# Performance work log

Hardware: AMD Instinct MI355X
Metric: run time of the kernel (lower is better)

The kernel has to match this reference:

```python
import math
import jax, jax.numpy as jnp
import numpy as np

B, S, D, H, REL_V = 2, 2048, 1024, 16, 64
HD = D // H
EPS = 1e-5


def _layernorm(x, w, b):
    # torch-style: std with Bessel correction (unbiased), divide by (std + eps)
    u = x.mean(-1, keepdims=True)
    xc = x - u
    s = jnp.sqrt((xc * xc).sum(-1, keepdims=True) / (x.shape[-1] - 1))
    return w * (xc / (s + EPS)) + b


def _gelu(x):
    return 0.5 * x * (1 + jnp.tanh(math.sqrt(2 / math.pi) * (x + 0.044715 * x ** 3)))


def setup_inputs() -> dict:
    key = jax.random.key(0)
    ks = jax.random.split(key, 6)
    wscale = 0.02
    return {
        "x": jax.random.normal(ks[0], (B, S, D), jnp.float32),
        "rel": jax.random.randint(ks[1], (B, S, S), 0, REL_V, jnp.int32),
        "ln1_w": jnp.ones((D,), jnp.float32),
        "ln1_b": jnp.zeros((D,), jnp.float32),
        "Wqkv": jax.random.normal(ks[2], (D, 3 * D), jnp.float32) * wscale,
        "bqkv": jnp.zeros((3 * D,), jnp.float32),
        "Wo": jax.random.normal(ks[3], (D, D), jnp.float32) * wscale,
        "bo": jnp.zeros((D,), jnp.float32),
        "rel_emb": jax.random.normal(ks[4], (REL_V, H), jnp.float32) * wscale,
        "ln2_w": jnp.ones((D,), jnp.float32),
        "ln2_b": jnp.zeros((D,), jnp.float32),
        "Wfc": jax.random.normal(ks[5], (D, 4 * D), jnp.float32) * wscale,
        "bfc": jnp.zeros((4 * D,), jnp.float32),
        "Wp": jax.random.normal(jax.random.fold_in(key, 7), (4 * D, D), jnp.float32) * wscale,
        "bp": jnp.zeros((D,), jnp.float32),
    }


def reference(x, rel, ln1_w, ln1_b, Wqkv, bqkv, Wo, bo, rel_emb,
              ln2_w, ln2_b, Wfc, bfc, Wp, bp):
    h = _layernorm(x, ln1_w, ln1_b)
    qkv = h @ Wqkv + bqkv  # [B,S,3D]
    q, k, v = jnp.split(qkv, 3, axis=-1)
    q = q.reshape(B, S, H, HD).transpose(0, 2, 1, 3)  # [B,H,S,HD]
    k = k.reshape(B, S, H, HD).transpose(0, 2, 1, 3)
    v = v.reshape(B, S, H, HD).transpose(0, 2, 1, 3)

    w = jnp.einsum('bhqd,bhkd->bhqk', q, k) / math.sqrt(HD)  # scale=True
    mask = jnp.tril(jnp.ones((S, S), w.dtype))  # causal tril buffer
    w = w * mask - 1e10 * (1 - mask)
    # faithful to original: rel bias multiplies masked logits (zeroing masked -1e10)
    relw = rel_emb[rel]                    # [B,S,S,H]
    relw = relw.transpose(0, 3, 1, 2)      # [B,H,S,S]
    w = w * (relw * mask)
    p = jax.nn.softmax(w, axis=-1)
    a = jnp.einsum('bhqk,bhkd->bhqd', p, v)       # [B,H,S,HD]
    a = a.transpose(0, 2, 1, 3).reshape(B, S, D)  # merge heads
    a = a @ Wo + bo

    x = x + a
    m = _gelu(_layernorm(x, ln2_w, ln2_b) @ Wfc + bfc) @ Wp + bp
    return x + m
```

## Files before the change

kernel.cpp:

```cpp
#include <hip/hip_runtime.h>
#include <hip/hip_bf16.h>
#include <math.h>

using bf16 = __hip_bfloat16;
typedef __bf16 bf16x8 __attribute__((ext_vector_type(8)));
typedef float f32x4 __attribute__((ext_vector_type(4)));

#define SEQ 2048
#define DIM 1024
#define NH 16
#define HDIM 64
#define BATCH 2

__device__ __forceinline__ void load_lds16(const bf16* g, bf16* l) {
  __builtin_amdgcn_global_load_lds((__attribute__((address_space(1))) void*)g,
                                   (__attribute__((address_space(3))) void*)l, 16, 0, 0);
}

__global__ __launch_bounds__(256) void transpose_k(const float* __restrict__ in,
                                                   bf16* __restrict__ out, int R, int C) {
  __shared__ float tile[32][33];
  int c0 = blockIdx.x * 32, r0 = blockIdx.y * 32;
  int tx = threadIdx.x, ty = threadIdx.y;
#pragma unroll
  for (int j = 0; j < 4; ++j)
    tile[ty + 8 * j][tx] = in[(size_t)(r0 + ty + 8 * j) * C + c0 + tx];
  __syncthreads();
#pragma unroll
  for (int j = 0; j < 4; ++j)
    out[(size_t)(c0 + ty + 8 * j) * R + r0 + tx] = __float2bfloat16(tile[tx][ty + 8 * j]);
}

__global__ __launch_bounds__(256) void ln_k(const float* __restrict__ x,
                                            const float* __restrict__ w,
                                            const float* __restrict__ bb,
                                            bf16* __restrict__ out) {
  int row = blockIdx.x, tid = threadIdx.x;
  int wid = tid >> 6, lane = tid & 63;
  const float* xr = x + (size_t)row * DIM;
  float4 vv = *(const float4*)&xr[tid * 4];
  float v[4] = {vv.x, vv.y, vv.z, vv.w};
  float s = v[0] + v[1] + v[2] + v[3];
#pragma unroll
  for (int m = 1; m < 64; m <<= 1) s += __shfl_xor(s, m, 64);
  __shared__ float red[8];
  if (lane == 0) red[wid] = s;
  __syncthreads();
  float mean = (red[0] + red[1] + red[2] + red[3]) * (1.f / DIM);
  float q = 0.f;
#pragma unroll
  for (int j = 0; j < 4; ++j) {
    v[j] -= mean;
    q += v[j] * v[j];
  }
#pragma unroll
  for (int m = 1; m < 64; m <<= 1) q += __shfl_xor(q, m, 64);
  if (lane == 0) red[4 + wid] = q;
  __syncthreads();
  float ssq = red[4] + red[5] + red[6] + red[7];
  float sd = sqrtf(ssq / (float)(DIM - 1));
  float inv = 1.f / (sd + 1e-5f);
  float4 wv = *(const float4*)&w[tid * 4];
  float4 bv4 = *(const float4*)&bb[tid * 4];
  float wl[4] = {wv.x, wv.y, wv.z, wv.w};
  float bl[4] = {bv4.x, bv4.y, bv4.z, bv4.w};
  unsigned short pk[4];
#pragma unroll
  for (int j = 0; j < 4; ++j)
    pk[j] = __bfloat16_as_ushort(__float2bfloat16(wl[j] * (v[j] * inv) + bl[j]));
  *(uint2*)&out[(size_t)row * DIM + tid * 4] = *(uint2*)pk;
}

__global__ __launch_bounds__(512) void gemm256_k(
    const bf16* __restrict__ A, const bf16* __restrict__ Bt, const float* __restrict__ bias,
    int N, int K, int mode, bf16* __restrict__ o0, bf16* __restrict__ o1,
    bf16* __restrict__ o2) {
  __shared__ bf16 LDSb[65536];
  int tid = threadIdx.x;
  int wid = tid >> 6, lane = tid & 63, quad = lane >> 4, l15 = lane & 15;
  int wm = wid >> 2, wn = wid & 3;
  int m0 = blockIdx.y * 256, n0 = blockIdx.x * 256;
  int grow = lane >> 2;
  int gslot = (lane & 3) ^ ((lane >> 3) & 3);
  const int nt = K >> 6;

  float bv[4];
#pragma unroll
  for (int nf = 0; nf < 4; ++nf) bv[nf] = bias[n0 + wn * 64 + nf * 16 + l15];

  auto stageA = [&](int tile, int ks) {
    int bd = tile & 1;
#pragma unroll
    for (int it = 0; it < 2; ++it) {
      int c = wid * 2 + it;
      load_lds16(A + (size_t)(m0 + c * 16 + grow) * K + tile * 64 + ks * 32 + gslot * 8,
                 &LDSb[bd * 32768 + ks * 8192 + c * 512]);
    }
  };
  auto stageB = [&](int tile, int ks) {
    int bd = tile & 1;
#pragma unroll
    for (int it = 0; it < 2; ++it) {
      int c = wid * 2 + it;
      load_lds16(Bt + (size_t)(n0 + c * 16 + grow) * K + tile * 64 + ks * 32 + gslot * 8,
                 &LDSb[bd * 32768 + 16384 + ks * 8192 + c * 512]);
    }
  };

  f32x4 acc[8][4] = {};

  stageA(0, 0); stageB(0, 0);
  stageA(0, 1); stageB(0, 1);
  stageA(1, 0); stageB(1, 0);
  asm volatile("s_waitcnt vmcnt(8)" ::: "memory");
  __builtin_amdgcn_sched_barrier(0);
  __builtin_amdgcn_s_barrier();
  __builtin_amdgcn_sched_barrier(0);

#define PHASE(BD, KS, MH, STAGE_STMT, WAIT_STMT)                                             \
  {                                                                                          \
    bf16x8 af[4], bq[4];                                                                     \
    _Pragma("unroll") for (int j = 0; j < 4; ++j) {                                          \
      int r = wm * 128 + (MH) * 64 + j * 16 + l15;                                           \
      af[j] = *(const bf16x8*)&LDSb[(BD) * 32768 + (KS) * 8192 + (r >> 4) * 512 +            \
                                    (r & 15) * 32 + ((quad ^ ((r >> 1) & 3)) << 3)];         \
    }                                                                                        \
    _Pragma("unroll") for (int n = 0; n < 4; ++n) {                                          \
      int r = wn * 64 + n * 16 + l15;                                                        \
      bq[n] = *(const bf16x8*)&LDSb[(BD) * 32768 + 16384 + (KS) * 8192 + (r >> 4) * 512 +    \
                                    (r & 15) * 32 + ((quad ^ ((r >> 1) & 3)) << 3)];         \
    }                                                                                        \
    STAGE_STMT;                                                                              \
    __builtin_amdgcn_sched_barrier(0);                                                       \
    __builtin_amdgcn_s_barrier();                                                            \
    __builtin_amdgcn_sched_barrier(0);                                                       \
    __builtin_amdgcn_s_setprio(1);                                                           \
    _Pragma("unroll") for (int j = 0; j < 4; ++j)                                            \
        _Pragma("unroll") for (int n = 0; n < 4; ++n)                                        \
            acc[(MH) * 4 + j][n] = __builtin_amdgcn_mfma_f32_16x16x32_bf16(                  \
                af[j], bq[n], acc[(MH) * 4 + j][n], 0, 0, 0);                                \
    __builtin_amdgcn_s_setprio(0);                                                           \
    WAIT_STMT;                                                                               \
    __builtin_amdgcn_sched_barrier(0);                                                       \
    __builtin_amdgcn_s_barrier();                                                            \
    __builtin_amdgcn_sched_barrier(0);                                                       \
  }

  for (int t = 0; t < nt; ++t) {
    int bd = t & 1;
    PHASE(bd, 0, 0, { if (t + 1 < nt) stageA(t + 1, 1); }, {});
    PHASE(bd, 0, 1, { if (t + 1 < nt) stageB(t + 1, 1); }, {
      if (t + 1 < nt) asm volatile("s_waitcnt vmcnt(8)" ::: "memory");
      else            asm volatile("s_waitcnt vmcnt(0)" ::: "memory");
    });
    PHASE(bd, 1, 0, { if (t + 2 < nt) stageA(t + 2, 0); }, {});
    PHASE(bd, 1, 1, { if (t + 2 < nt) stageB(t + 2, 0); }, {
      if (t + 2 < nt)      asm volatile("s_waitcnt vmcnt(8)" ::: "memory");
      else if (t + 1 < nt) asm volatile("s_waitcnt vmcnt(4)" ::: "memory");
    });
  }
#undef PHASE

#pragma unroll
  for (int mf = 0; mf < 8; ++mf) {
#pragma unroll
    for (int nf = 0; nf < 4; ++nf) {
      int col = n0 + wn * 64 + nf * 16 + l15;
      int row_base = m0 + wm * 128 + mf * 16 + quad * 4;
      if (mode == 0) {
        int which = col >> 10, d = col & 1023, hh = d >> 6, dd = d & 63;
        int b = row_base >> 11, s2 = row_base & 2047;
        if (which == 2) {
          unsigned short pk[4];
#pragma unroll
          for (int r = 0; r < 4; ++r)
            pk[r] = __bfloat16_as_ushort(__float2bfloat16(acc[mf][nf][r] + bv[nf]));
          *(uint2*)&o2[(((size_t)b * NH + hh) * HDIM + dd) * SEQ + s2] = *(uint2*)pk;
        } else {
          bf16* dst = which == 0 ? o0 : o1;
#pragma unroll
          for (int r = 0; r < 4; ++r)
            dst[(((size_t)b * NH + hh) * SEQ + s2 + r) * HDIM + dd] =
                __float2bfloat16(acc[mf][nf][r] + bv[nf]);
        }
      } else {
#pragma unroll
        for (int r = 0; r < 4; ++r) {
          float t2 = acc[mf][nf][r] + bv[nf];
          float u = 0.7978845608028654f * (t2 + 0.044715f * t2 * t2 * t2);
          float g = t2 / (1.f + __expf(-2.f * u));
          o0[(size_t)(row_base + r) * N + col] = __float2bfloat16(g);
        }
      }
    }
  }
}

template <int TM>
__global__ __launch_bounds__(256) void gemm_k(
    const bf16* __restrict__ A, const bf16* __restrict__ Bt, const float* __restrict__ bias,
    int M, int N, int K, int mode,
    const float* __restrict__ residf, float* __restrict__ x2out, const float* __restrict__ x2in,
    float* __restrict__ outf) {
  constexpr int MT = TM / 32;
  constexpr int ACH = TM / 8;
  __shared__ bf16 As[TM * 64];
  __shared__ bf16 Bs[128 * 64];
  int tid = threadIdx.x;
  int wid = tid >> 6, lane = tid & 63, quad = lane >> 4, l15 = lane & 15;
  int wm = wid >> 1, wn = wid & 1;
  int m0 = blockIdx.y * TM, n0 = blockIdx.x * 128;
  int rsub = lane >> 3;
  int c8 = (lane & 7) ^ rsub;
  f32x4 acc[MT][4] = {};

  for (int k0 = 0; k0 < K; k0 += 64) {
    __syncthreads();
#pragma unroll
    for (int it = 0; it < ACH / 4; ++it) {
      int c = wid * (ACH / 4) + it;
      int row = c * 8 + rsub;
      load_lds16(A + (size_t)(m0 + row) * K + k0 + c8 * 8, &As[c * 512]);
    }
#pragma unroll
    for (int it = 0; it < 4; ++it) {
      int c = wid * 4 + it;
      int row = c * 8 + rsub;
      load_lds16(Bt + (size_t)(n0 + row) * K + k0 + c8 * 8, &Bs[c * 512]);
    }
    __syncthreads();
#pragma unroll
    for (int ks = 0; ks < 2; ++ks) {
      bf16x8 af[MT], bfr[4];
#pragma unroll
      for (int mt = 0; mt < MT; ++mt) {
        int r = wm * (MT * 16) + mt * 16 + l15;
        af[mt] = *(const bf16x8*)&As[r * 64 + ((ks * 4 + quad) ^ (r & 7)) * 8];
      }
#pragma unroll
      for (int nt2 = 0; nt2 < 4; ++nt2) {
        int r = wn * 64 + nt2 * 16 + l15;
        bfr[nt2] = *(const bf16x8*)&Bs[r * 64 + ((ks * 4 + quad) ^ (r & 7)) * 8];
      }
#pragma unroll
      for (int mt = 0; mt < MT; ++mt)
#pragma unroll
        for (int nt2 = 0; nt2 < 4; ++nt2)
          acc[mt][nt2] =
              __builtin_amdgcn_mfma_f32_16x16x32_bf16(af[mt], bfr[nt2], acc[mt][nt2], 0, 0, 0);
    }
  }

#pragma unroll
  for (int mt = 0; mt < MT; ++mt) {
#pragma unroll
    for (int nt = 0; nt < 4; ++nt) {
      int col = n0 + wn * 64 + nt * 16 + l15;
      float bvs = bias[col];
      int row_base = m0 + wm * (MT * 16) + mt * 16 + quad * 4;
#pragma unroll
      for (int r = 0; r < 4; ++r) {
        int row = row_base + r;
        float val = acc[mt][nt][r] + bvs;
        size_t i = (size_t)row * N + col;
        if (mode == 1) x2out[i] = residf[i] + val;
        else           outf[i] = x2in[i] + val;
      }
    }
  }
}

__global__ __launch_bounds__(256) void sufv_k(const bf16* __restrict__ vt,
                                              float* __restrict__ suf) {
  int row = blockIdx.x;
  const bf16* src = vt + (size_t)row * SEQ;
  float* dst = suf + (size_t)row * SEQ;
  int tid = threadIdx.x;
  float v[8];
  float s = 0.f;
#pragma unroll
  for (int j = 0; j < 8; ++j) {
    v[j] = __bfloat162float(src[tid * 8 + j]);
    s += v[j];
  }
  __shared__ float sc[256];
  sc[tid] = s;
  __syncthreads();
  for (int off = 1; off < 256; off <<= 1) {
    float add = (tid + off < 256) ? sc[tid + off] : 0.f;
    __syncthreads();
    sc[tid] += add;
    __syncthreads();
  }
  float run = (tid < 255) ? sc[tid + 1] : 0.f;
#pragma unroll
  for (int j = 7; j >= 0; --j) {
    dst[tid * 8 + j] = run;
    run += v[j];
  }
}

__device__ __forceinline__ int pswz(int row) { return (row & 7) ^ (((row >> 3) & 1) << 1); }

__global__ __launch_bounds__(256) void attn_k(const bf16* __restrict__ q,
                                              const bf16* __restrict__ k,
                                              const bf16* __restrict__ v,
                                              const int* __restrict__ rel,
                                              const float* __restrict__ rel_emb,
                                              const float* __restrict__ suf,
                                              bf16* __restrict__ out) {
  int h = blockIdx.x;
  int y = blockIdx.y;
  int b = blockIdx.z;
  int tid = threadIdx.x;
  int wid = tid >> 6, lane = tid & 63, quad = lane >> 4, l15 = lane & 15;

  __shared__ __align__(16) char SM[40960];
  bf16* Kb = (bf16*)SM;
  bf16* Vb = (bf16*)(SM + 16384);
  bf16* Ps = (bf16*)(SM + 32768);
  float(*SufLds)[68] = (float(*)[68])SM;

  const size_t bh = (size_t)b * NH + h;
  const bf16* kb0 = k + bh * SEQ * HDIM;
  const bf16* vt0 = v + bh * (size_t)HDIM * SEQ;

  float rv = 0.125f * rel_emb[lane * NH + h];

  int rsub = lane >> 3;
  int c8 = (lane & 7) ^ rsub;

  const int prow_w = wid * 16 + quad * 4;
  const int prow_r = wid * 16 + l15;
  const int psw_r = pswz(prow_r);

  for (int sub = 0; sub < 2; ++sub) {
    int qt = (sub == 0) ? (31 - y) : y;

    const bf16* qb = q + (bh * SEQ + (size_t)qt * 64) * HDIM;
    bf16x8 aq[2];
#pragma unroll
    for (int ks = 0; ks < 2; ++ks)
      aq[ks] = *(const bf16x8*)(qb + (size_t)(wid * 16 + l15) * HDIM + ks * 32 + quad * 8);

    __syncthreads();

#pragma unroll
    for (int it = 0; it < 2; ++it) {
      int c = wid * 2 + it;
      int row = c * 8 + rsub;
      load_lds16(kb0 + (size_t)row * HDIM + c8 * 8, &Kb[c * 512]);
      load_lds16(vt0 + (size_t)row * SEQ + c8 * 8, &Vb[c * 512]);
    }

    const int* relq = rel + (size_t)b * SEQ * SEQ + (size_t)qt * 64 * SEQ;
    const int* rp[4];
#pragma unroll
    for (int r = 0; r < 4; ++r) rp[r] = relq + (size_t)(wid * 16 + quad * 4 + r) * SEQ;

    int ridx[4][4];
#pragma unroll
    for (int nt = 0; nt < 4; ++nt)
#pragma unroll
      for (int r = 0; r < 4; ++r) ridx[nt][r] = rp[r][nt * 16 + l15];

    __syncthreads();

    const int q_base = qt * 64 + wid * 16 + quad * 4;
    float l_part[4] = {0.f, 0.f, 0.f, 0.f};
    f32x4 o_acc[4] = {};

    for (int kt = 0; kt < qt; ++kt) {
      int cur = kt & 1;
      int ridx2[4][4];
      {
        bf16* Kd = Kb + (cur ^ 1) * 4096;
        bf16* Vd = Vb + (cur ^ 1) * 4096;
#pragma unroll
        for (int it = 0; it < 2; ++it) {
          int c = wid * 2 + it;
          int row = c * 8 + rsub;
          load_lds16(kb0 + (size_t)((kt + 1) * 64 + row) * HDIM + c8 * 8, &Kd[c * 512]);
          load_lds16(vt0 + (size_t)row * SEQ + (kt + 1) * 64 + c8 * 8, &Vd[c * 512]);
        }
#pragma unroll
        for (int nt = 0; nt < 4; ++nt)
#pragma unroll
          for (int r = 0; r < 4; ++r) ridx2[nt][r] = rp[r][(kt + 1) * 64 + nt * 16 + l15];
      }

      const bf16* Ksb = Kb + cur * 4096;
      const bf16* Vtb = Vb + cur * 4096;

      f32x4 sacc[4] = {};
      __builtin_amdgcn_s_setprio(1);
#pragma unroll
      for (int ks = 0; ks < 2; ++ks) {
#pragma unroll
        for (int nt = 0; nt < 4; ++nt) {
          bf16x8 bfr =
              *(const bf16x8*)&Ksb[(nt * 16 + l15) * 64 + ((ks * 4 + quad) ^ (l15 & 7)) * 8];
          sacc[nt] = __builtin_amdgcn_mfma_f32_16x16x32_bf16(aq[ks], bfr, sacc[nt], 0, 0, 0);
        }
      }
      __builtin_amdgcn_s_setprio(0);

#pragma unroll
      for (int nt = 0; nt < 4; ++nt) {
#pragma unroll
        for (int r = 0; r < 4; ++r) {
          float m = __shfl(rv, ridx[nt][r], 64);
          float p = __expf(sacc[nt][r] * m);
          l_part[r] += p;
          int row = prow_w + r;
          int sw = (nt * 2 + (l15 >> 3)) ^ pswz(row);
          Ps[row * 64 + sw * 8 + (l15 & 7)] = __float2bfloat16(p);
        }
      }

      __builtin_amdgcn_s_setprio(1);
#pragma unroll
      for (int ks = 0; ks < 2; ++ks) {
        bf16x8 af = *(const bf16x8*)&Ps[prow_r * 64 + ((ks * 4 + quad) ^ psw_r) * 8];
#pragma unroll
        for (int nt = 0; nt < 4; ++nt) {
          bf16x8 bfr =
              *(const bf16x8*)&Vtb[(nt * 16 + l15) * 64 + ((ks * 4 + quad) ^ (l15 & 7)) * 8];
          o_acc[nt] = __builtin_amdgcn_mfma_f32_16x16x32_bf16(af, bfr, o_acc[nt], 0, 0, 0);
        }
      }
      __builtin_amdgcn_s_setprio(0);

      __syncthreads();

#pragma unroll
      for (int nt = 0; nt < 4; ++nt)
#pragma unroll
        for (int r = 0; r < 4; ++r) ridx[nt][r] = ridx2[nt][r];
    }

    {
      int cur = qt & 1;
      const bf16* Ksb = Kb + cur * 4096;
      const bf16* Vtb = Vb + cur * 4096;

      f32x4 sacc[4] = {};
      __builtin_amdgcn_s_setprio(1);
#pragma unroll
      for (int ks = 0; ks < 2; ++ks) {
#pragma unroll
        for (int nt = 0; nt < 4; ++nt) {
          bf16x8 bfr =
              *(const bf16x8*)&Ksb[(nt * 16 + l15) * 64 + ((ks * 4 + quad) ^ (l15 & 7)) * 8];
          sacc[nt] = __builtin_amdgcn_mfma_f32_16x16x32_bf16(aq[ks], bfr, sacc[nt], 0, 0, 0);
        }
      }
      __builtin_amdgcn_s_setprio(0);

#pragma unroll
      for (int nt = 0; nt < 4; ++nt) {
#pragma unroll
        for (int r = 0; r < 4; ++r) {
          float m = __shfl(rv, ridx[nt][r], 64);
          float p = __expf(sacc[nt][r] * m);
          int k_abs = qt * 64 + nt * 16 + l15;
          if (k_abs > q_base + r) p = 0.f;
          l_part[r] += p;
          int row = prow_w + r;
          int sw = (nt * 2 + (l15 >> 3)) ^ pswz(row);
          Ps[row * 64 + sw * 8 + (l15 & 7)] = __float2bfloat16(p);
        }
      }

      __builtin_amdgcn_s_setprio(1);
#pragma unroll
      for (int ks = 0; ks < 2; ++ks) {
        bf16x8 af = *(const bf16x8*)&Ps[prow_r * 64 + ((ks * 4 + quad) ^ psw_r) * 8];
#pragma unroll
        for (int nt = 0; nt < 4; ++nt) {
          bf16x8 bfr =
              *(const bf16x8*)&Vtb[(nt * 16 + l15) * 64 + ((ks * 4 + quad) ^ (l15 & 7)) * 8];
          o_acc[nt] = __builtin_amdgcn_mfma_f32_16x16x32_bf16(af, bfr, o_acc[nt], 0, 0, 0);
        }
      }
      __builtin_amdgcn_s_setprio(0);

      __syncthreads();
    }

#pragma unroll
    for (int r = 0; r < 4; ++r)
#pragma unroll
      for (int m = 1; m < 16; m <<= 1) l_part[r] += __shfl_xor(l_part[r], m, 64);

    const float* sufb = suf + bh * (size_t)HDIM * SEQ + (size_t)qt * 64;
#pragma unroll
    for (int p = 0; p < 4; ++p) {
      int idx = p * 256 + tid;
      int d = idx >> 4, qq = idx & 15;
      *(float4*)&SufLds[d][qq * 4] = *(const float4*)(sufb + (size_t)d * SEQ + qq * 4);
    }
    __syncthreads();

#pragma unroll
    for (int nt = 0; nt < 4; ++nt) {
      int d = nt * 16 + l15;
#pragma unroll
      for (int r = 0; r < 4; ++r) {
        int row = q_base + r;
        int cnt = (SEQ - 1) - row;
        float l = l_part[r] + (float)cnt;
        int q_local = wid * 16 + quad * 4 + r;
        float ov = (o_acc[nt][r] + SufLds[d][q_local]) / l;
        out[((size_t)b * SEQ + row) * DIM + h * HDIM + d] = __float2bfloat16(ov);
      }
    }
  }
}

extern "C" void kernel_launch(void* const* d_in, const int* in_sizes, int n_in,
                              void* d_out, int out_size, void* d_ws, size_t ws_size,
                              hipStream_t stream) {
  const float* x = (const float*)d_in[0];
  const int* rel = (const int*)d_in[1];
  const float* ln1w = (const float*)d_in[2];
  const float* ln1b = (const float*)d_in[3];
  const float* Wqkv = (const float*)d_in[4];
  const float* bqkv = (const float*)d_in[5];
  const float* Wo = (const float*)d_in[6];
  const float* bo = (const float*)d_in[7];
  const float* rel_emb = (const float*)d_in[8];
  const float* ln2w = (const float*)d_in[9];
  const float* ln2b = (const float*)d_in[10];
  const float* Wfc = (const float*)d_in[11];
  const float* bfc = (const float*)d_in[12];
  const float* Wp = (const float*)d_in[13];
  const float* bp = (const float*)d_in[14];
  float* outp = (float*)d_out;

  char* ws = (char*)d_ws;
  const size_t MB = 1u << 20;
  bf16* h = (bf16*)(ws + 0);
  bf16* qb = (bf16*)(ws + 8 * MB);
  bf16* kb = (bf16*)(ws + 16 * MB);
  bf16* vb = (bf16*)(ws + 24 * MB);
  float* x2 = (float*)(ws + 32 * MB);
  float* suf = (float*)(ws + 32 * MB);
  bf16* fcb = (bf16*)(ws + 48 * MB);
  bf16* wqkvT = (bf16*)(ws + 48 * MB);
  bf16* woT = (bf16*)(ws + 54 * MB);
  bf16* wfcT = (bf16*)(ws + 16 * MB);
  bf16* wpT = (bf16*)(ws + 24 * MB);

  dim3 tb(32, 8);
  transpose_k<<<dim3(3072 / 32, 1024 / 32), tb, 0, stream>>>(Wqkv, wqkvT, 1024, 3072);
  transpose_k<<<dim3(1024 / 32, 1024 / 32), tb, 0, stream>>>(Wo, woT, 1024, 1024);

  ln_k<<<BATCH * SEQ, 256, 0, stream>>>(x, ln1w, ln1b, h);

  gemm256_k<<<dim3(3072 / 256, 4096 / 256), 512, 0, stream>>>(
      h, wqkvT, bqkv, 3072, 1024, 0, qb, kb, vb);

  sufv_k<<<BATCH * NH * HDIM, 256, 0, stream>>>(vb, suf);

  attn_k<<<dim3(NH, 16, BATCH), 256, 0, stream>>>(qb, kb, vb, rel, rel_emb, suf, h);

  gemm_k<64><<<dim3(1024 / 128, 4096 / 64), 256, 0, stream>>>(
      h, woT, bo, BATCH * SEQ, 1024, 1024, 1, x, x2, nullptr, nullptr);

  transpose_k<<<dim3(4096 / 32, 1024 / 32), tb, 0, stream>>>(Wfc, wfcT, 1024, 4096);
  transpose_k<<<dim3(1024 / 32, 4096 / 32), tb, 0, stream>>>(Wp, wpT, 4096, 1024);

  ln_k<<<BATCH * SEQ, 256, 0, stream>>>(x2, ln2w, ln2b, qb);

  gemm256_k<<<dim3(4096 / 256, 4096 / 256), 512, 0, stream>>>(
      qb, wfcT, bfc, 4096, 1024, 2, fcb, nullptr, nullptr);

  gemm_k<64><<<dim3(1024 / 128, 4096 / 64), 256, 0, stream>>>(
      fcb, wpT, bp, BATCH * SEQ, 1024, 4096, 3, nullptr, nullptr, x2, outp);
}
```

Measured before the change: 404.6 us.

## Replace narrow output GEMMs with split-K 256-tile GEMM using atomic accumulation

```diff
diff --git a/kernel.cpp b/kernel.cpp
--- a/kernel.cpp
+++ b/kernel.cpp
@@ -34,11 +34,19 @@
 __global__ __launch_bounds__(256) void ln_k(const float* __restrict__ x,
                                             const float* __restrict__ w,
                                             const float* __restrict__ bb,
-                                            bf16* __restrict__ out) {
+                                            bf16* __restrict__ out,
+                                            const float* __restrict__ addb,
+                                            float* __restrict__ initout) {
   int row = blockIdx.x, tid = threadIdx.x;
   int wid = tid >> 6, lane = tid & 63;
   const float* xr = x + (size_t)row * DIM;
   float4 vv = *(const float4*)&xr[tid * 4];
+  if (initout) {
+    float4 ab = *(const float4*)&addb[tid * 4];
+    float4 iv;
+    iv.x = vv.x + ab.x; iv.y = vv.y + ab.y; iv.z = vv.z + ab.z; iv.w = vv.w + ab.w;
+    *(float4*)&initout[(size_t)row * DIM + tid * 4] = iv;
+  }
   float v[4] = {vv.x, vv.y, vv.z, vv.w};
   float s = v[0] + v[1] + v[2] + v[3];
 #pragma unroll
@@ -73,8 +81,8 @@
 
 __global__ __launch_bounds__(512) void gemm256_k(
     const bf16* __restrict__ A, const bf16* __restrict__ Bt, const float* __restrict__ bias,
-    int N, int K, int mode, bf16* __restrict__ o0, bf16* __restrict__ o1,
-    bf16* __restrict__ o2) {
+    int N, int Kstride, int klen, int mode, bf16* __restrict__ o0, bf16* __restrict__ o1,
+    bf16* __restrict__ o2, float* __restrict__ fdst) {
   __shared__ bf16 LDSb[65536];
   int tid = threadIdx.x;
   int wid = tid >> 6, lane = tid & 63, quad = lane >> 4, l15 = lane & 15;
@@ -82,19 +90,23 @@
   int m0 = blockIdx.y * 256, n0 = blockIdx.x * 256;
   int grow = lane >> 2;
   int gslot = (lane & 3) ^ ((lane >> 3) & 3);
-  const int nt = K >> 6;
-
-  float bv[4];
-#pragma unroll
-  for (int nf = 0; nf < 4; ++nf) bv[nf] = bias[n0 + wn * 64 + nf * 16 + l15];
+  const int nt = klen >> 6;
+  const int kOff = blockIdx.z * klen;
+
+  float bv[4] = {0.f, 0.f, 0.f, 0.f};
+  if (bias) {
+#pragma unroll
+    for (int nf = 0; nf < 4; ++nf) bv[nf] = bias[n0 + wn * 64 + nf * 16 + l15];
+  }
 
   auto stageA = [&](int tile, int ks) {
     int bd = tile & 1;
 #pragma unroll
     for (int it = 0; it < 2; ++it) {
       int c = wid * 2 + it;
-      load_lds16(A + (size_t)(m0 + c * 16 + grow) * K + tile * 64 + ks * 32 + gslot * 8,
-                 &LDSb[bd * 32768 + ks * 8192 + c * 512]);
+      load_lds16(
+          A + (size_t)(m0 + c * 16 + grow) * Kstride + kOff + tile * 64 + ks * 32 + gslot * 8,
+          &LDSb[bd * 32768 + ks * 8192 + c * 512]);
     }
   };
   auto stageB = [&](int tile, int ks) {
@@ -102,8 +114,9 @@
 #pragma unroll
     for (int it = 0; it < 2; ++it) {
       int c = wid * 2 + it;
-      load_lds16(Bt + (size_t)(n0 + c * 16 + grow) * K + tile * 64 + ks * 32 + gslot * 8,
-                 &LDSb[bd * 32768 + 16384 + ks * 8192 + c * 512]);
+      load_lds16(
+          Bt + (size_t)(n0 + c * 16 + grow) * Kstride + kOff + tile * 64 + ks * 32 + gslot * 8,
+          &LDSb[bd * 32768 + 16384 + ks * 8192 + c * 512]);
     }
   };
 
@@ -183,7 +196,7 @@
             dst[(((size_t)b * NH + hh) * SEQ + s2 + r) * HDIM + dd] =
                 __float2bfloat16(acc[mf][nf][r] + bv[nf]);
         }
-      } else {
+      } else if (mode == 2) {
 #pragma unroll
         for (int r = 0; r < 4; ++r) {
           float t2 = acc[mf][nf][r] + bv[nf];
@@ -191,80 +204,10 @@
           float g = t2 / (1.f + __expf(-2.f * u));
           o0[(size_t)(row_base + r) * N + col] = __float2bfloat16(g);
         }
-      }
-    }
-  }
-}
-
-template <int TM>
-__global__ __launch_bounds__(256) void gemm_k(
-    const bf16* __restrict__ A, const bf16* __restrict__ Bt, const float* __restrict__ bias,
-    int M, int N, int K, int mode,
-    const float* __restrict__ residf, float* __restrict__ x2out, const float* __restrict__ x2in,
-    float* __restrict__ outf) {
-  constexpr int MT = TM / 32;
-  constexpr int ACH = TM / 8;
-  __shared__ bf16 As[TM * 64];
-  __shared__ bf16 Bs[128 * 64];
-  int tid = threadIdx.x;
-  int wid = tid >> 6, lane = tid & 63, quad = lane >> 4, l15 = lane & 15;
-  int wm = wid >> 1, wn = wid & 1;
-  int m0 = blockIdx.y * TM, n0 = blockIdx.x * 128;
-  int rsub = lane >> 3;
-  int c8 = (lane & 7) ^ rsub;
-  f32x4 acc[MT][4] = {};
-
-  for (int k0 = 0; k0 < K; k0 += 64) {
-    __syncthreads();
-#pragma unroll
-    for (int it = 0; it < ACH / 4; ++it) {
-      int c = wid * (ACH / 4) + it;
-      int row = c * 8 + rsub;
-      load_lds16(A + (size_t)(m0 + row) * K + k0 + c8 * 8, &As[c * 512]);
-    }
-#pragma unroll
-    for (int it = 0; it < 4; ++it) {
-      int c = wid * 4 + it;
-      int row = c * 8 + rsub;
-      load_lds16(Bt + (size_t)(n0 + row) * K + k0 + c8 * 8, &Bs[c * 512]);
-    }
-    __syncthreads();
-#pragma unroll
-    for (int ks = 0; ks < 2; ++ks) {
-      bf16x8 af[MT], bfr[4];
-#pragma unroll
-      for (int mt = 0; mt < MT; ++mt) {
-        int r = wm * (MT * 16) + mt * 16 + l15;
-        af[mt] = *(const bf16x8*)&As[r * 64 + ((ks * 4 + quad) ^ (r & 7)) * 8];
-      }
-#pragma unroll
-      for (int nt2 = 0; nt2 < 4; ++nt2) {
-        int r = wn * 64 + nt2 * 16 + l15;
-        bfr[nt2] = *(const bf16x8*)&Bs[r * 64 + ((ks * 4 + quad) ^ (r & 7)) * 8];
-      }
-#pragma unroll
-      for (int mt = 0; mt < MT; ++mt)
-#pragma unroll
-        for (int nt2 = 0; nt2 < 4; ++nt2)
-          acc[mt][nt2] =
-              __builtin_amdgcn_mfma_f32_16x16x32_bf16(af[mt], bfr[nt2], acc[mt][nt2], 0, 0, 0);
-    }
-  }
-
-#pragma unroll
-  for (int mt = 0; mt < MT; ++mt) {
-#pragma unroll
-    for (int nt = 0; nt < 4; ++nt) {
-      int col = n0 + wn * 64 + nt * 16 + l15;
-      float bvs = bias[col];
-      int row_base = m0 + wm * (MT * 16) + mt * 16 + quad * 4;
-#pragma unroll
-      for (int r = 0; r < 4; ++r) {
-        int row = row_base + r;
-        float val = acc[mt][nt][r] + bvs;
-        size_t i = (size_t)row * N + col;
-        if (mode == 1) x2out[i] = residf[i] + val;
-        else           outf[i] = x2in[i] + val;
+      } else {
+#pragma unroll
+        for (int r = 0; r < 4; ++r)
+          atomicAdd(&fdst[(size_t)(row_base + r) * N + col], acc[mf][nf][r]);
       }
     }
   }
@@ -308,7 +251,10 @@
                                               const int* __restrict__ rel,
                                               const float* __restrict__ rel_emb,
                                               const float* __restrict__ suf,
-                                              bf16* __restrict__ out) {
+                                              bf16* __restrict__ out,
+                                              const float* __restrict__ xin,
+                                              const float* __restrict__ bo_,
+                                              float* __restrict__ x2f) {
   int h = blockIdx.x;
   int y = blockIdx.y;
   int b = blockIdx.z;
@@ -333,6 +279,10 @@
   const int prow_w = wid * 16 + quad * 4;
   const int prow_r = wid * 16 + l15;
   const int psw_r = pswz(prow_r);
+
+  float bov[4];
+#pragma unroll
+  for (int nt = 0; nt < 4; ++nt) bov[nt] = bo_[h * HDIM + nt * 16 + l15];
 
   for (int sub = 0; sub < 2; ++sub) {
     int qt = (sub == 0) ? (31 - y) : y;
@@ -512,7 +462,9 @@
         float l = l_part[r] + (float)cnt;
         int q_local = wid * 16 + quad * 4 + r;
         float ov = (o_acc[nt][r] + SufLds[d][q_local]) / l;
-        out[((size_t)b * SEQ + row) * DIM + h * HDIM + d] = __float2bfloat16(ov);
+        size_t oidx = ((size_t)b * SEQ + row) * DIM + h * HDIM + d;
+        out[oidx] = __float2bfloat16(ov);
+        x2f[oidx] = xin[oidx] + bov[nt];
       }
     }
   }
@@ -543,39 +495,39 @@
   bf16* h = (bf16*)(ws + 0);
   bf16* qb = (bf16*)(ws + 8 * MB);
   bf16* kb = (bf16*)(ws + 16 * MB);
+  bf16* wpT = (bf16*)(ws + 16 * MB);
   bf16* vb = (bf16*)(ws + 24 * MB);
-  float* x2 = (float*)(ws + 32 * MB);
+  bf16* wfcT = (bf16*)(ws + 24 * MB);
   float* suf = (float*)(ws + 32 * MB);
-  bf16* fcb = (bf16*)(ws + 48 * MB);
-  bf16* wqkvT = (bf16*)(ws + 48 * MB);
-  bf16* woT = (bf16*)(ws + 54 * MB);
-  bf16* wfcT = (bf16*)(ws + 16 * MB);
-  bf16* wpT = (bf16*)(ws + 24 * MB);
+  bf16* wqkvT = (bf16*)(ws + 49 * MB);
+  bf16* woT = (bf16*)(ws + 55 * MB);
+  float* x2 = (float*)(ws + 57 * MB);
+  bf16* fcb = (bf16*)(ws + 32 * MB);
 
   dim3 tb(32, 8);
   transpose_k<<<dim3(3072 / 32, 1024 / 32), tb, 0, stream>>>(Wqkv, wqkvT, 1024, 3072);
   transpose_k<<<dim3(1024 / 32, 1024 / 32), tb, 0, stream>>>(Wo, woT, 1024, 1024);
 
-  ln_k<<<BATCH * SEQ, 256, 0, stream>>>(x, ln1w, ln1b, h);
-
-  gemm256_k<<<dim3(3072 / 256, 4096 / 256), 512, 0, stream>>>(
-      h, wqkvT, bqkv, 3072, 1024, 0, qb, kb, vb);
+  ln_k<<<BATCH * SEQ, 256, 0, stream>>>(x, ln1w, ln1b, h, nullptr, nullptr);
+
+  gemm256_k<<<dim3(3072 / 256, 4096 / 256, 1), 512, 0, stream>>>(
+      h, wqkvT, bqkv, 3072, 1024, 1024, 0, qb, kb, vb, nullptr);
 
   sufv_k<<<BATCH * NH * HDIM, 256, 0, stream>>>(vb, suf);
 
-  attn_k<<<dim3(NH, 16, BATCH), 256, 0, stream>>>(qb, kb, vb, rel, rel_emb, suf, h);
-
-  gemm_k<64><<<dim3(1024 / 128, 4096 / 64), 256, 0, stream>>>(
-      h, woT, bo, BATCH * SEQ, 1024, 1024, 1, x, x2, nullptr, nullptr);
+  attn_k<<<dim3(NH, 16, BATCH), 256, 0, stream>>>(qb, kb, vb, rel, rel_emb, suf, h, x, bo, x2);
+
+  gemm256_k<<<dim3(1024 / 256, 4096 / 256, 4), 512, 0, stream>>>(
+      h, woT, nullptr, 1024, 1024, 256, 4, nullptr, nullptr, nullptr, x2);
 
   transpose_k<<<dim3(4096 / 32, 1024 / 32), tb, 0, stream>>>(Wfc, wfcT, 1024, 4096);
   transpose_k<<<dim3(1024 / 32, 4096 / 32), tb, 0, stream>>>(Wp, wpT, 4096, 1024);
 
-  ln_k<<<BATCH * SEQ, 256, 0, stream>>>(x2, ln2w, ln2b, qb);
-
-  gemm256_k<<<dim3(4096 / 256, 4096 / 256), 512, 0, stream>>>(
-      qb, wfcT, bfc, 4096, 1024, 2, fcb, nullptr, nullptr);
-
-  gemm_k<64><<<dim3(1024 / 128, 4096 / 64), 256, 0, stream>>>(
-      fcb, wpT, bp, BATCH * SEQ, 1024, 4096, 3, nullptr, nullptr, x2, outp);
-}
+  ln_k<<<BATCH * SEQ, 256, 0, stream>>>(x2, ln2w, ln2b, qb, bp, outp);
+
+  gemm256_k<<<dim3(4096 / 256, 4096 / 256, 1), 512, 0, stream>>>(
+      qb, wfcT, bfc, 4096, 1024, 1024, 2, fcb, nullptr, nullptr, nullptr);
+
+  gemm256_k<<<dim3(1024 / 256, 4096 / 256, 4), 512, 0, stream>>>(
+      fcb, wpT, nullptr, 1024, 4096, 1024, 4, nullptr, nullptr, nullptr, outp);
+}
```

Result: slower. 487.5 us (+20.5%).

## Split-K the MLP down projection on the 256-tile GEMM with atomic accumulation

Applied to the files above, without the earlier changes.

```diff
diff --git a/kernel.cpp b/kernel.cpp
--- a/kernel.cpp
+++ b/kernel.cpp
@@ -34,11 +34,19 @@
 __global__ __launch_bounds__(256) void ln_k(const float* __restrict__ x,
                                             const float* __restrict__ w,
                                             const float* __restrict__ bb,
-                                            bf16* __restrict__ out) {
+                                            bf16* __restrict__ out,
+                                            const float* __restrict__ addb,
+                                            float* __restrict__ initout) {
   int row = blockIdx.x, tid = threadIdx.x;
   int wid = tid >> 6, lane = tid & 63;
   const float* xr = x + (size_t)row * DIM;
   float4 vv = *(const float4*)&xr[tid * 4];
+  if (initout) {
+    float4 ab = *(const float4*)&addb[tid * 4];
+    float4 iv;
+    iv.x = vv.x + ab.x; iv.y = vv.y + ab.y; iv.z = vv.z + ab.z; iv.w = vv.w + ab.w;
+    *(float4*)&initout[(size_t)row * DIM + tid * 4] = iv;
+  }
   float v[4] = {vv.x, vv.y, vv.z, vv.w};
   float s = v[0] + v[1] + v[2] + v[3];
 #pragma unroll
@@ -73,8 +81,8 @@
 
 __global__ __launch_bounds__(512) void gemm256_k(
     const bf16* __restrict__ A, const bf16* __restrict__ Bt, const float* __restrict__ bias,
-    int N, int K, int mode, bf16* __restrict__ o0, bf16* __restrict__ o1,
-    bf16* __restrict__ o2) {
+    int N, int Kstride, int klen, int mode, bf16* __restrict__ o0, bf16* __restrict__ o1,
+    bf16* __restrict__ o2, float* __restrict__ fdst) {
   __shared__ bf16 LDSb[65536];
   int tid = threadIdx.x;
   int wid = tid >> 6, lane = tid & 63, quad = lane >> 4, l15 = lane & 15;
@@ -82,19 +90,23 @@
   int m0 = blockIdx.y * 256, n0 = blockIdx.x * 256;
   int grow = lane >> 2;
   int gslot = (lane & 3) ^ ((lane >> 3) & 3);
-  const int nt = K >> 6;
-
-  float bv[4];
-#pragma unroll
-  for (int nf = 0; nf < 4; ++nf) bv[nf] = bias[n0 + wn * 64 + nf * 16 + l15];
+  const int nt = klen >> 6;
+  const int kOff = blockIdx.z * klen;
+
+  float bv[4] = {0.f, 0.f, 0.f, 0.f};
+  if (bias) {
+#pragma unroll
+    for (int nf = 0; nf < 4; ++nf) bv[nf] = bias[n0 + wn * 64 + nf * 16 + l15];
+  }
 
   auto stageA = [&](int tile, int ks) {
     int bd = tile & 1;
 #pragma unroll
     for (int it = 0; it < 2; ++it) {
       int c = wid * 2 + it;
-      load_lds16(A + (size_t)(m0 + c * 16 + grow) * K + tile * 64 + ks * 32 + gslot * 8,
-                 &LDSb[bd * 32768 + ks * 8192 + c * 512]);
+      load_lds16(
+          A + (size_t)(m0 + c * 16 + grow) * Kstride + kOff + tile * 64 + ks * 32 + gslot * 8,
+          &LDSb[bd * 32768 + ks * 8192 + c * 512]);
     }
   };
   auto stageB = [&](int tile, int ks) {
@@ -102,8 +114,9 @@
 #pragma unroll
     for (int it = 0; it < 2; ++it) {
       int c = wid * 2 + it;
-      load_lds16(Bt + (size_t)(n0 + c * 16 + grow) * K + tile * 64 + ks * 32 + gslot * 8,
-                 &LDSb[bd * 32768 + 16384 + ks * 8192 + c * 512]);
+      load_lds16(
+          Bt + (size_t)(n0 + c * 16 + grow) * Kstride + kOff + tile * 64 + ks * 32 + gslot * 8,
+          &LDSb[bd * 32768 + 16384 + ks * 8192 + c * 512]);
     }
   };
 
@@ -183,7 +196,7 @@
             dst[(((size_t)b * NH + hh) * SEQ + s2 + r) * HDIM + dd] =
                 __float2bfloat16(acc[mf][nf][r] + bv[nf]);
         }
-      } else {
+      } else if (mode == 2) {
 #pragma unroll
         for (int r = 0; r < 4; ++r) {
           float t2 = acc[mf][nf][r] + bv[nf];
@@ -191,6 +204,10 @@
           float g = t2 / (1.f + __expf(-2.f * u));
           o0[(size_t)(row_base + r) * N + col] = __float2bfloat16(g);
         }
+      } else {
+#pragma unroll
+        for (int r = 0; r < 4; ++r)
+          atomicAdd(&fdst[(size_t)(row_base + r) * N + col], acc[mf][nf][r]);
       }
     }
   }
@@ -543,23 +560,23 @@
   bf16* h = (bf16*)(ws + 0);
   bf16* qb = (bf16*)(ws + 8 * MB);
   bf16* kb = (bf16*)(ws + 16 * MB);
+  bf16* wpT = (bf16*)(ws + 16 * MB);
   bf16* vb = (bf16*)(ws + 24 * MB);
-  float* x2 = (float*)(ws + 32 * MB);
+  bf16* wfcT = (bf16*)(ws + 24 * MB);
   float* suf = (float*)(ws + 32 * MB);
-  bf16* fcb = (bf16*)(ws + 48 * MB);
-  bf16* wqkvT = (bf16*)(ws + 48 * MB);
-  bf16* woT = (bf16*)(ws + 54 * MB);
-  bf16* wfcT = (bf16*)(ws + 16 * MB);
-  bf16* wpT = (bf16*)(ws + 24 * MB);
+  bf16* wqkvT = (bf16*)(ws + 49 * MB);
+  bf16* woT = (bf16*)(ws + 55 * MB);
+  float* x2 = (float*)(ws + 57 * MB);
+  bf16* fcb = (bf16*)(ws + 32 * MB);
 
   dim3 tb(32, 8);
   transpose_k<<<dim3(3072 / 32, 1024 / 32), tb, 0, stream>>>(Wqkv, wqkvT, 1024, 3072);
   transpose_k<<<dim3(1024 / 32, 1024 / 32), tb, 0, stream>>>(Wo, woT, 1024, 1024);
 
-  ln_k<<<BATCH * SEQ, 256, 0, stream>>>(x, ln1w, ln1b, h);
-
-  gemm256_k<<<dim3(3072 / 256, 4096 / 256), 512, 0, stream>>>(
-      h, wqkvT, bqkv, 3072, 1024, 0, qb, kb, vb);
+  ln_k<<<BATCH * SEQ, 256, 0, stream>>>(x, ln1w, ln1b, h, nullptr, nullptr);
+
+  gemm256_k<<<dim3(3072 / 256, 4096 / 256, 1), 512, 0, stream>>>(
+      h, wqkvT, bqkv, 3072, 1024, 1024, 0, qb, kb, vb, nullptr);
 
   sufv_k<<<BATCH * NH * HDIM, 256, 0, stream>>>(vb, suf);
 
@@ -571,11 +588,11 @@
   transpose_k<<<dim3(4096 / 32, 1024 / 32), tb, 0, stream>>>(Wfc, wfcT, 1024, 4096);
   transpose_k<<<dim3(1024 / 32, 4096 / 32), tb, 0, stream>>>(Wp, wpT, 4096, 1024);
 
-  ln_k<<<BATCH * SEQ, 256, 0, stream>>>(x2, ln2w, ln2b, qb);
-
-  gemm256_k<<<dim3(4096 / 256, 4096 / 256), 512, 0, stream>>>(
-      qb, wfcT, bfc, 4096, 1024, 2, fcb, nullptr, nullptr);
-
-  gemm_k<64><<<dim3(1024 / 128, 4096 / 64), 256, 0, stream>>>(
-      fcb, wpT, bp, BATCH * SEQ, 1024, 4096, 3, nullptr, nullptr, x2, outp);
-}
+  ln_k<<<BATCH * SEQ, 256, 0, stream>>>(x2, ln2w, ln2b, qb, bp, outp);
+
+  gemm256_k<<<dim3(4096 / 256, 4096 / 256, 1), 512, 0, stream>>>(
+      qb, wfcT, bfc, 4096, 1024, 1024, 2, fcb, nullptr, nullptr, nullptr);
+
+  gemm256_k<<<dim3(1024 / 256, 4096 / 256, 4), 512, 0, stream>>>(
+      fcb, wpT, nullptr, 1024, 4096, 1024, 4, nullptr, nullptr, nullptr, outp);
+}
```

After: 434.5 us. +7.4%, slower.
